# Kernel optimization log

Measured on AMD Instinct MI355X. Metric: run time of the kernel, lower is better.

Reference implementation:

```python
import jax, jax.numpy as jnp
import numpy as np

H = 32          # num_attention_heads
HD = 128        # head_dim
HID = H * HD    # hidden_size = 4096
KB_LEN = 1024   # number of KB entries
TOPK = 128      # top_k_kb (dynamic_sparsify=True)
ROPE_THETA = 10000.0
PAD = -1000000000.0  # PADDING_VALUE


def rope_cos_sin(position_ids, head_dim, theta):
    inv_freq = 1.0 / (theta ** (jnp.arange(0, head_dim, 2, dtype=jnp.float32) / head_dim))
    freqs = position_ids.astype(jnp.float32)[..., None] * inv_freq  # [B,q,hd/2]
    emb = jnp.concatenate([freqs, freqs], axis=-1)                  # [B,q,hd]
    return jnp.cos(emb), jnp.sin(emb)


def rotate_half(x):
    half = x.shape[-1] // 2
    return jnp.concatenate([-x[..., half:], x[..., :half]], axis=-1)


def apply_rope(q, k, cos, sin):
    cos = cos[:, None]  # [B,1,q,hd]
    sin = sin[:, None]
    return q * cos + rotate_half(q) * sin, k * cos + rotate_half(k) * sin


def setup_inputs() -> dict:
    key = jax.random.key(0)
    ks = jax.random.split(key, 9)
    B, Q = 1, 2048
    w_scale = 0.02  # keep activations numerically sane
    hidden_states = jax.random.normal(ks[0], (B, Q, HID), jnp.float32)
    causal = jnp.where(jnp.tril(jnp.ones((Q, Q), bool)), 0.0, PAD).astype(jnp.float32)
    attention_mask = jnp.broadcast_to(causal[None, None], (B, 1, Q, Q))
    position_ids = jnp.broadcast_to(jnp.arange(Q)[None], (B, Q))
    kb_keys = jax.random.normal(ks[1], (KB_LEN, HID), jnp.float32)
    kb_values = jax.random.normal(ks[2], (KB_LEN, HID), jnp.float32)
    Wq = jax.random.normal(ks[3], (HID, HID), jnp.float32) * w_scale
    Wq2 = jax.random.normal(ks[4], (HID, HID), jnp.float32) * w_scale
    Wk = jax.random.normal(ks[5], (HID, HID), jnp.float32) * w_scale
    Wv = jax.random.normal(ks[6], (HID, HID), jnp.float32) * w_scale
    Wo = jax.random.normal(ks[7], (HID, HID), jnp.float32) * w_scale
    score_shift = jnp.zeros((H, 1), jnp.float32) - 3.0
    return {"hidden_states": hidden_states, "attention_mask": attention_mask,
            "position_ids": position_ids, "kb_keys": kb_keys, "kb_values": kb_values,
            "Wq": Wq, "Wq2": Wq2, "Wk": Wk, "Wv": Wv, "Wo": Wo,
            "score_shift": score_shift}


def kblam_attention(hidden_states, attention_mask, position_ids, kb_keys, kb_values,
                    Wq, Wq2, Wk, Wv, Wo, score_shift):
    B, Q, _ = hidden_states.shape
    scale = 1.0 / np.sqrt(HD)

    def heads(x):  # [B,Q,HID] -> [B,H,Q,HD]
        return x.reshape(B, Q, H, HD).transpose(0, 2, 1, 3)

    q = heads(hidden_states @ Wq.T)
    q2 = heads(hidden_states @ Wq2.T)   # second query head (used for KB top-k pruning)
    k = heads(hidden_states @ Wk.T)
    v = heads(hidden_states @ Wv.T)

    cos, sin = rope_cos_sin(position_ids, HD, ROPE_THETA)
    q, k = apply_rope(q, k, cos, sin)   # num_kv_groups == 1, repeat_kv is identity

    # --- KB path: [kb_len, H*HD] -> [B,H,kb_len,HD] ---
    kbk = jnp.broadcast_to(kb_keys.reshape(KB_LEN, H, HD).transpose(1, 0, 2)[None], (B, H, KB_LEN, HD))
    kbv = jnp.broadcast_to(kb_values.reshape(KB_LEN, H, HD).transpose(1, 0, 2)[None], (B, H, KB_LEN, HD))

    # prune_key_value (dynamic_sparsify): top-k KB rows by summed q2-scores
    aw2 = jnp.einsum('bhqd,bhkd->bhqk', q2, kbk) * scale          # [B,H,Q,KB_LEN]
    idx = jax.lax.stop_gradient(jax.lax.top_k(aw2.sum((1, 2)), TOPK)[1])  # [B,TOPK]
    gidx = jnp.broadcast_to(idx[:, None, :, None], (B, H, TOPK, HD))
    kbk = jnp.take_along_axis(kbk, gidx, axis=2)                  # [B,H,TOPK,HD]
    kbv = jnp.take_along_axis(kbv, gidx, axis=2)
    kb_len = TOPK

    k_all = jnp.concatenate([kbk, k], axis=2)                     # [B,H,kb_len+Q,HD]
    v_all = jnp.concatenate([kbv, v], axis=2)

    # kb attention mask: zeros, except fully-padded query rows get PADDING_VALUE
    padding_mask = jnp.all(attention_mask < 0, axis=-1, keepdims=True)  # [B,1,Q,1]
    kb_mask = jnp.where(padding_mask, PAD, 0.0).astype(attention_mask.dtype)
    mask = jnp.concatenate([jnp.broadcast_to(kb_mask, (B, 1, Q, kb_len)), attention_mask], axis=-1)

    attn = jnp.einsum('bhqd,bhkd->bhqk', q, k_all) * scale
    # learned per-head shift on KB scores (score_shift: [H,1], init -3)
    attn = attn.at[..., :kb_len].add(score_shift.reshape(1, H, 1, 1))
    attn = attn + mask
    attn = jax.nn.softmax(attn.astype(jnp.float32), axis=-1).astype(q.dtype)

    out = jnp.einsum('bhqk,bhkd->bhqd', attn, v_all)              # [B,H,Q,HD]
    out = out.transpose(0, 2, 1, 3).reshape(B, Q, HID)
    return out @ Wo.T


def reference(hidden_states, attention_mask, position_ids, kb_keys, kb_values,
              Wq, Wq2, Wk, Wv, Wo, score_shift):
    return kblam_attention(hidden_states, attention_mask, position_ids, kb_keys, kb_values,
                           Wq, Wq2, Wk, Wv, Wo, score_shift)
```

## Files before the change

### kernel.cpp

```cpp
#include <hip/hip_runtime.h>
#include <stdint.h>
#include <stddef.h>

#define NH 32
#define HD 128
#define HID 4096
#define QLEN 2048
#define KBLEN 1024
#define NTOPK 128
#define KVLEN 2176
#define PADV -1e9f
#define SCALE 0.08838834764831845f
#define LOG2E 1.4426950408889634f
#define SC2 (SCALE * LOG2E)
#define DEFER_THR 8.0f

typedef __attribute__((ext_vector_type(4))) float f32x4;
typedef __attribute__((ext_vector_type(4))) unsigned short u16x4;
typedef __attribute__((ext_vector_type(8))) short s16x8;
typedef __attribute__((ext_vector_type(4))) short s16x4;

typedef const __attribute__((address_space(1))) void* gas1_t;
typedef __attribute__((address_space(3))) void* las3_t;

__device__ __forceinline__ void gload_lds16(const void* g, void* l) {
  __builtin_amdgcn_global_load_lds((gas1_t)g, (las3_t)l, 16, 0, 0);
}

__device__ __forceinline__ unsigned short f2bf(float x) {
  union { float f; unsigned u; } z; z.f = x;
  unsigned r = z.u + 0x7fffu + ((z.u >> 16) & 1u);
  return (unsigned short)(r >> 16);
}

__device__ __forceinline__ s16x4 tr16(unsigned addr) {
  s16x4 r;
  asm volatile("ds_read_b64_tr_b16 %0, %1" : "=v"(r) : "v"(addr));
  return r;
}

__device__ __forceinline__ s16x8 cat8(s16x4 a, s16x4 b) {
  s16x8 r;
  r[0]=a[0]; r[1]=a[1]; r[2]=a[2]; r[3]=a[3];
  r[4]=b[0]; r[5]=b[1]; r[6]=b[2]; r[7]=b[3];
  return r;
}


__global__ void k_cast(const float* __restrict__ src, unsigned short* __restrict__ dst, int n4) {
  int i = blockIdx.x * 256 + threadIdx.x;
  if (i >= n4) return;
  f32x4 v = ((const f32x4*)src)[i];
  u16x4 o;
  o[0] = f2bf(v[0]); o[1] = f2bf(v[1]); o[2] = f2bf(v[2]); o[3] = f2bf(v[3]);
  ((u16x4*)dst)[i] = o;
}

__global__ void k_rowsum_p(const float* __restrict__ x, float* __restrict__ part) {
  int d = blockIdx.x * 256 + threadIdx.x;
  int q0 = blockIdx.y * 128;
  float acc = 0.f;
  for (int q = q0; q < q0 + 128; ++q) acc += x[(size_t)q * HID + d];
  part[(size_t)blockIdx.y * HID + d] = acc;
}
__global__ void k_rowsum_r(const float* __restrict__ part, float* __restrict__ out) {
  int d = blockIdx.x * 256 + threadIdx.x;
  float acc = 0.f;
#pragma unroll
  for (int i = 0; i < 16; ++i) acc += part[(size_t)i * HID + d];
  out[d] = acc;
}

__global__ void k_dotrows(const float* __restrict__ vec, const float* __restrict__ mat,
                          float* __restrict__ out, int K, float s) {
  int n = blockIdx.x * 4 + (threadIdx.x >> 6);
  int lane = threadIdx.x & 63;
  const float* row = mat + (size_t)n * K;
  float acc = 0.f;
  for (int j = lane; j < K; j += 64) acc += vec[j] * row[j];
#pragma unroll
  for (int off = 32; off > 0; off >>= 1) acc += __shfl_down(acc, off, 64);
  if (lane == 0) out[n] = acc * s;
}

__global__ void k_topk(const float* __restrict__ scores, int* __restrict__ idx) {
  __shared__ float s[KBLEN];
  int t = threadIdx.x;
  s[t] = scores[t];
  __syncthreads();
  float mine = s[t];
  int rank = 0;
  for (int j = 0; j < KBLEN; ++j) {
    float v = s[j];
    rank += (v > mine) || (v == mine && j < t);
  }
  if (rank < NTOPK) idx[rank] = t;
}

__global__ void k_cs(const int* __restrict__ pos_ids, float2* __restrict__ cs) {
  int t = blockIdx.x * 256 + threadIdx.x;
  int p = t >> 6, i = t & 63;
  float pos = (float)pos_ids[p];
  float invf = powf(10000.0f, -(float)i / 64.0f);
  float a = pos * invf;
  cs[p * 64 + i] = make_float2(cosf(a), sinf(a));
}

__global__ void k_gather(const float* __restrict__ kbk, const float* __restrict__ kbv,
                         const int* __restrict__ idx,
                         unsigned short* __restrict__ kall, unsigned short* __restrict__ vall) {
  int t = blockIdx.x * 256 + threadIdx.x;
  int d = t & 127;
  int i = (t >> 7) & 127;
  int hh = t >> 14;
  int kr = idx[i];
  size_t src = (size_t)kr * HID + hh * HD + d;
  size_t dstoff = ((size_t)hh * KVLEN + i) * HD + d;
  kall[dstoff] = f2bf(kbk[src]);
  vall[dstoff] = f2bf(kbv[src]);
}

#define GBK 64
#define ABUF 8192
#define BBUF 16384
#define BUFE (ABUF + BBUF)

template<int MODE>
__global__ __launch_bounds__(512)
void gemm_bt(const unsigned short* __restrict__ A, const unsigned short* __restrict__ B,
             float* __restrict__ Cf, unsigned short* __restrict__ Cb,
             int M, int N, int K, int RH, int RO, const float2* __restrict__ cs2) {
  __shared__ unsigned short lds[3 * BUFE];
  const int tid = threadIdx.x;
  const int lane = tid & 63;
  const int wave = tid >> 6;
  const int lo = lane & 15, hi = lane >> 4;
  const int wm = wave >> 2, wn = wave & 3;

  const int nwg = gridDim.x * gridDim.y;
  const int orig = blockIdx.y * gridDim.x + blockIdx.x;
  const int wg = (orig & 7) * (nwg >> 3) + (orig >> 3);
  const int bx = wg % gridDim.x, by = wg / gridDim.x;
  const int m0 = by * 128, n0 = bx * 256;

  auto stageA = [&](int kt, int bufe, int g) {
    int j0 = g * 512 + wave * 64;
    int j = j0 + lane;
    int row = j >> 3, cb = j & 7;
    gload_lds16(A + (size_t)(m0 + row) * K + kt * GBK + ((cb ^ (row & 7)) << 3),
                (void*)(lds + bufe + j0 * 8));
  };
  auto stageB = [&](int kt, int bufe, int g) {
    int j0 = g * 512 + wave * 64;
    int j = j0 + lane;
    int row = j >> 3, cb = j & 7;
    gload_lds16(B + (size_t)(n0 + row) * K + kt * GBK + ((cb ^ (row & 7)) << 3),
                (void*)(lds + bufe + ABUF + j0 * 8));
  };

  f32x4 acc[4][4] = {};

  stageA(0, 0, 0); stageA(0, 0, 1);
  stageB(0, 0, 0); stageB(0, 0, 1); stageB(0, 0, 2); stageB(0, 0, 3);
  stageA(1, BUFE, 0); stageA(1, BUFE, 1);
  stageB(1, BUFE, 0); stageB(1, BUFE, 1); stageB(1, BUFE, 2); stageB(1, BUFE, 3);

  const int NT = K / GBK;
  const int sa = (lo & 7) << 3;
  const int bbase = (wn >> 1) * 128 + (wn & 1) * 32;
  int bi = 0;

  for (int kt = 0; kt < NT; ++kt) {
    if (kt < NT - 1) { asm volatile("s_waitcnt vmcnt(6)" ::: "memory"); }
    else             { asm volatile("s_waitcnt vmcnt(0)" ::: "memory"); }
    __builtin_amdgcn_sched_barrier(0);
    __builtin_amdgcn_s_barrier();
    __builtin_amdgcn_sched_barrier(0);

    const int bufe = bi * BUFE;
    const int nbufe = ((bi + 2 >= 3) ? bi - 1 : bi + 2) * BUFE;
    const bool pre = (kt + 2 < NT);
    const unsigned short* Ab = lds + bufe;
    const unsigned short* Bb = lds + bufe + ABUF;
    const int arow = wm * 64 + lo;
    const int brow = bbase + lo;

    s16x8 af[4], b01[2], b23[2];
    const int c0 = (hi * 8) ^ sa;
    const int c1 = (32 + hi * 8) ^ sa;

#pragma unroll
    for (int i = 0; i < 4; ++i) af[i] = *(const s16x8*)(Ab + (arow + i * 16) * 64 + c0);
    b01[0] = *(const s16x8*)(Bb + (brow +  0) * 64 + c0);
    b01[1] = *(const s16x8*)(Bb + (brow + 16) * 64 + c0);
    if (pre) { stageA(kt + 2, nbufe, 0); stageA(kt + 2, nbufe, 1); }
    asm volatile("s_waitcnt lgkmcnt(0)" ::: "memory");
    __builtin_amdgcn_sched_barrier(0);
    __builtin_amdgcn_s_setprio(1);
#pragma unroll
    for (int i = 0; i < 4; ++i) {
      acc[i][0] = __builtin_amdgcn_mfma_f32_16x16x32_bf16(af[i], b01[0], acc[i][0], 0, 0, 0);
      acc[i][1] = __builtin_amdgcn_mfma_f32_16x16x32_bf16(af[i], b01[1], acc[i][1], 0, 0, 0);
    }
    __builtin_amdgcn_s_setprio(0);

    b23[0] = *(const s16x8*)(Bb + (brow + 64) * 64 + c0);
    b23[1] = *(const s16x8*)(Bb + (brow + 80) * 64 + c0);
    if (pre) { stageB(kt + 2, nbufe, 0); stageB(kt + 2, nbufe, 1); }
    asm volatile("s_waitcnt lgkmcnt(0)" ::: "memory");
    __builtin_amdgcn_sched_barrier(0);
    __builtin_amdgcn_s_setprio(1);
#pragma unroll
    for (int i = 0; i < 4; ++i) {
      acc[i][2] = __builtin_amdgcn_mfma_f32_16x16x32_bf16(af[i], b23[0], acc[i][2], 0, 0, 0);
      acc[i][3] = __builtin_amdgcn_mfma_f32_16x16x32_bf16(af[i], b23[1], acc[i][3], 0, 0, 0);
    }
    __builtin_amdgcn_s_setprio(0);

#pragma unroll
    for (int i = 0; i < 4; ++i) af[i] = *(const s16x8*)(Ab + (arow + i * 16) * 64 + c1);
    b01[0] = *(const s16x8*)(Bb + (brow +  0) * 64 + c1);
    b01[1] = *(const s16x8*)(Bb + (brow + 16) * 64 + c1);
    if (pre) { stageB(kt + 2, nbufe, 2); stageB(kt + 2, nbufe, 3); }
    asm volatile("s_waitcnt lgkmcnt(0)" ::: "memory");
    __builtin_amdgcn_sched_barrier(0);
    __builtin_amdgcn_s_setprio(1);
#pragma unroll
    for (int i = 0; i < 4; ++i) {
      acc[i][0] = __builtin_amdgcn_mfma_f32_16x16x32_bf16(af[i], b01[0], acc[i][0], 0, 0, 0);
      acc[i][1] = __builtin_amdgcn_mfma_f32_16x16x32_bf16(af[i], b01[1], acc[i][1], 0, 0, 0);
    }
    __builtin_amdgcn_s_setprio(0);

    b23[0] = *(const s16x8*)(Bb + (brow + 64) * 64 + c1);
    b23[1] = *(const s16x8*)(Bb + (brow + 80) * 64 + c1);
    asm volatile("s_waitcnt lgkmcnt(0)" ::: "memory");
    __builtin_amdgcn_sched_barrier(0);
    __builtin_amdgcn_s_setprio(1);
#pragma unroll
    for (int i = 0; i < 4; ++i) {
      acc[i][2] = __builtin_amdgcn_mfma_f32_16x16x32_bf16(af[i], b23[0], acc[i][2], 0, 0, 0);
      acc[i][3] = __builtin_amdgcn_mfma_f32_16x16x32_bf16(af[i], b23[1], acc[i][3], 0, 0, 0);
    }
    __builtin_amdgcn_s_setprio(0);

    bi = (bi + 1 == 3) ? 0 : bi + 1;
  }

  if (MODE == 2) {
#pragma unroll
    for (int i = 0; i < 4; ++i) {
#pragma unroll
      for (int j = 0; j < 2; ++j) {
#pragma unroll
        for (int r = 0; r < 4; ++r) {
          int row = m0 + wm * 64 + i * 16 + hi * 4 + r;
          int col = n0 + bbase + j * 16 + lo;
          int hh = col >> 7, d = col & 127;
          float2 cp = cs2[row * 64 + d];
          float x1 = acc[i][j][r], x2 = acc[i][j + 2][r];
          size_t base = ((size_t)hh * RH + RO + row) * HD;
          Cb[base + d]      = f2bf(x1 * cp.x - x2 * cp.y);
          Cb[base + d + 64] = f2bf(x2 * cp.x + x1 * cp.y);
        }
      }
    }
  } else {
#pragma unroll
    for (int i = 0; i < 4; ++i) {
#pragma unroll
      for (int j = 0; j < 4; ++j) {
#pragma unroll
        for (int r = 0; r < 4; ++r) {
          int row = m0 + wm * 64 + i * 16 + hi * 4 + r;
          int col = n0 + bbase + (j >> 1) * 64 + (j & 1) * 16 + lo;
          float v = acc[i][j][r];
          if (MODE == 0) {
            Cf[(size_t)row * N + col] = v;
          } else {
            int hh = col >> 7, d = col & 127;
            Cb[((size_t)hh * RH + RO + row) * HD + d] = f2bf(v);
          }
        }
      }
    }
  }
}

__global__ __launch_bounds__(256)
void attn_kernel(const unsigned short* __restrict__ qh,
                 const unsigned short* __restrict__ kall,
                 const unsigned short* __restrict__ vall,
                 const float* __restrict__ sshift,
                 unsigned short* __restrict__ ctx) {
  __shared__ __align__(1024) unsigned short Ks[2][64 * 128];
  __shared__ __align__(1024) unsigned short Vs[2][64 * 128];
  __shared__ __align__(16)  unsigned short Plds[4][16 * 72];

  int orig = blockIdx.y * 16 + blockIdx.x;
  int wgid = (orig & 7) * 64 + (orig >> 3);
  int h = wgid >> 4;
  int xch = wgid & 15;

  const int tid = threadIdx.x;
  const int lane = tid & 63;
  const int wave = tid >> 6;
  const int lo = lane & 15;
  const int hi = lane >> 4;
  const float shiftL = sshift[h] * LOG2E;

  const unsigned short* kb = kall + (size_t)h * KVLEN * HD;
  const unsigned short* vb = vall + (size_t)h * KVLEN * HD;

#pragma unroll 1
  for (int half = 0; half < 2; ++half) {
    const int qc = half ? (31 - xch) : xch;
    const int m0 = qc * 64;

    s16x8 qf[4];
    {
      const unsigned short* qp = qh + ((size_t)h * QLEN + m0 + wave * 16 + lo) * HD + hi * 8;
#pragma unroll
      for (int kc = 0; kc < 4; ++kc) qf[kc] = *(const s16x8*)(qp + kc * 32);
    }

    float m_run[4], l_run[4];
#pragma unroll
    for (int r = 0; r < 4; ++r) { m_run[r] = -1e30f; l_run[r] = 0.f; }
    f32x4 o[8] = {};

    const int nt = qc + 3;
    const int qrow = m0 + wave * 16 + hi * 4;
    int buf = 0;

    auto STAGE = [&](int kt, int b) {
      const unsigned short* kg = kb + (size_t)kt * 64 * HD;
      const unsigned short* vg = vb + (size_t)kt * 64 * HD;
#pragma unroll
      for (int it = 0; it < 4; ++it) {
        int j0 = it * 256 + wave * 64;
        int j = j0 + lane;
        int row = j >> 4, cb = j & 15;
        gload_lds16(kg + row * 128 + ((cb ^ (row & 7)) * 8), (void*)(Ks[b] + j0 * 8));
        int kq = j >> 6, dc = (j >> 3) & 7, kr = (j >> 1) & 3, hf = j & 1;
        gload_lds16(vg + (kq * 4 + kr) * 128 + dc * 16 + hf * 8, (void*)(Vs[b] + j0 * 8));
      }
    };

    STAGE(0, 0);
    __syncthreads();

    for (int kt = 0; kt < nt; ++kt) {
      if (kt + 1 < nt) STAGE(kt + 1, buf ^ 1);

      f32x4 s[4] = {};
#pragma unroll
      for (int kc = 0; kc < 4; ++kc) {
#pragma unroll
        for (int g = 0; g < 4; ++g) {
          int key = g * 16 + lo;
          s16x8 kf = *(const s16x8*)(Ks[buf] + key * 128 + (((kc * 4 + hi) ^ (key & 7)) * 8));
          s[g] = __builtin_amdgcn_mfma_f32_16x16x32_bf16(qf[kc], kf, s[g], 0, 0, 0);
        }
      }

      const int kvbase = kt * 64;
      float sv[4][4], mx[4];
#pragma unroll
      for (int r = 0; r < 4; ++r) {
        int qr = qrow + r;
#pragma unroll
        for (int g = 0; g < 4; ++g) {
          int kv = kvbase + g * 16 + lo;
          float v = s[g][r] * SC2;
          v = (kv < NTOPK) ? (v + shiftL) : ((kv - NTOPK > qr) ? PADV : v);
          sv[g][r] = v;
        }
        mx[r] = fmaxf(fmaxf(sv[0][r], sv[1][r]), fmaxf(sv[2][r], sv[3][r]));
      }
#pragma unroll
      for (int off = 1; off < 16; off <<= 1)
#pragma unroll
        for (int r = 0; r < 4; ++r) mx[r] = fmaxf(mx[r], __shfl_xor(mx[r], off, 64));

      bool need = false;
#pragma unroll
      for (int r = 0; r < 4; ++r) need = need || (mx[r] > m_run[r] + DEFER_THR);
      if (need) {
#pragma unroll
        for (int r = 0; r < 4; ++r) {
          float mn = fmaxf(m_run[r], mx[r]);
          float alpha = __builtin_amdgcn_exp2f(m_run[r] - mn);
          m_run[r] = mn;
          l_run[r] *= alpha;
#pragma unroll
          for (int db = 0; db < 8; ++db) o[db][r] *= alpha;
        }
      }

      float rs[4];
#pragma unroll
      for (int r = 0; r < 4; ++r) {
        float acc = 0.f;
#pragma unroll
        for (int g = 0; g < 4; ++g) {
          float p = __builtin_amdgcn_exp2f(sv[g][r] - m_run[r]);
          acc += p;
          Plds[wave][(hi * 4 + r) * 72 + g * 16 + lo] = f2bf(p);
        }
        rs[r] = acc;
      }
#pragma unroll
      for (int off = 1; off < 16; off <<= 1)
#pragma unroll
        for (int r = 0; r < 4; ++r) rs[r] += __shfl_xor(rs[r], off, 64);
#pragma unroll
      for (int r = 0; r < 4; ++r) l_run[r] += rs[r];

      s16x8 pf0 = *(const s16x8*)(&Plds[wave][lo * 72 + hi * 8]);
      s16x8 pf1 = *(const s16x8*)(&Plds[wave][lo * 72 + 32 + hi * 8]);
      const unsigned vb0 = (unsigned)(uintptr_t)(&Vs[buf][0]) + hi * 2048 + lo * 8;
#pragma unroll
      for (int dbp = 0; dbp < 4; ++dbp) {
        s16x4 t[2][2][2];
#pragma unroll
        for (int dbi = 0; dbi < 2; ++dbi) {
          unsigned a0 = vb0 + (dbp * 2 + dbi) * 128;
          t[dbi][0][0] = tr16(a0);
          t[dbi][0][1] = tr16(a0 + 1024);
          t[dbi][1][0] = tr16(a0 + 8192);
          t[dbi][1][1] = tr16(a0 + 8192 + 1024);
        }
        asm volatile("s_waitcnt lgkmcnt(0)" ::: "memory");
        __builtin_amdgcn_sched_barrier(0);
#pragma unroll
        for (int dbi = 0; dbi < 2; ++dbi) {
          int db = dbp * 2 + dbi;
          o[db] = __builtin_amdgcn_mfma_f32_16x16x32_bf16(pf0, cat8(t[dbi][0][0], t[dbi][0][1]), o[db], 0, 0, 0);
          o[db] = __builtin_amdgcn_mfma_f32_16x16x32_bf16(pf1, cat8(t[dbi][1][0], t[dbi][1][1]), o[db], 0, 0, 0);
        }
      }

      __syncthreads();
      buf ^= 1;
    }

#pragma unroll
    for (int db = 0; db < 8; ++db) {
#pragma unroll
      for (int r = 0; r < 4; ++r) {
        int row = qrow + r;
        int col = h * HD + db * 16 + lo;
        ctx[(size_t)row * HID + col] = f2bf(o[db][r] / l_run[r]);
      }
    }
  }
}


extern "C" void kernel_launch(void* const* d_in, const int* in_sizes, int n_in,
                              void* d_out, int out_size, void* d_ws, size_t ws_size,
                              hipStream_t stream) {
  const float* hidden    = (const float*)d_in[0];
  const int*   pos       = (const int*)d_in[2];
  const float* kb_keys   = (const float*)d_in[3];
  const float* kb_values = (const float*)d_in[4];
  const float* Wq        = (const float*)d_in[5];
  const float* Wq2       = (const float*)d_in[6];
  const float* Wk        = (const float*)d_in[7];
  const float* Wv        = (const float*)d_in[8];
  const float* Wo        = (const float*)d_in[9];
  const float* sshift    = (const float*)d_in[10];
  float* out = (float*)d_out;

  char* ws = (char*)d_ws;
  size_t off = 0;
  auto alloc = [&](size_t bytes) { char* p = ws + off; off += (bytes + 255) & ~(size_t)255; return p; };
  unsigned short* hidden_bf = (unsigned short*)alloc((size_t)QLEN * HID * 2);
  unsigned short* wbuf      = (unsigned short*)alloc((size_t)HID * HID * 2);
  unsigned short* qbf       = (unsigned short*)alloc((size_t)NH * QLEN * HD * 2);
  unsigned short* kallp     = (unsigned short*)alloc((size_t)NH * KVLEN * HD * 2);
  unsigned short* vallp     = (unsigned short*)alloc((size_t)NH * KVLEN * HD * 2);
  unsigned short* ctx       = (unsigned short*)alloc((size_t)QLEN * HID * 2);
  float2*         cs2       = (float2*)alloc((size_t)QLEN * 64 * 8);
  float*          part      = (float*)alloc((size_t)16 * HID * 4);
  float*          hsum      = (float*)alloc(HID * 4);
  float*          qs        = (float*)alloc(HID * 4);
  float*          scores    = (float*)alloc(KBLEN * 4);
  int*            idx       = (int*)alloc(NTOPK * 4);

  dim3 blk(256);

  k_cast<<<QLEN * HID / 4 / 256, blk, 0, stream>>>(hidden, hidden_bf, QLEN * HID / 4);
  k_rowsum_p<<<dim3(HID / 256, 16), blk, 0, stream>>>(hidden, part);
  k_rowsum_r<<<HID / 256, blk, 0, stream>>>(part, hsum);
  k_dotrows<<<HID / 4, blk, 0, stream>>>(hsum, Wq2, qs, HID, 1.0f);
  k_dotrows<<<KBLEN / 4, blk, 0, stream>>>(qs, kb_keys, scores, HID, SCALE);
  k_topk<<<1, KBLEN, 0, stream>>>(scores, idx);
  k_cs<<<QLEN * 64 / 256, blk, 0, stream>>>(pos, cs2);

  dim3 ggrid(HID / 256, QLEN / 128);
  dim3 gblk(512);
  int wcast_blocks = HID * HID / 4 / 256;

  k_cast<<<wcast_blocks, blk, 0, stream>>>(Wq, wbuf, HID * HID / 4);
  gemm_bt<2><<<ggrid, gblk, 0, stream>>>(hidden_bf, wbuf, nullptr, qbf, QLEN, HID, HID, QLEN, 0, cs2);
  k_cast<<<wcast_blocks, blk, 0, stream>>>(Wk, wbuf, HID * HID / 4);
  gemm_bt<2><<<ggrid, gblk, 0, stream>>>(hidden_bf, wbuf, nullptr, kallp, QLEN, HID, HID, KVLEN, NTOPK, cs2);
  k_cast<<<wcast_blocks, blk, 0, stream>>>(Wv, wbuf, HID * HID / 4);
  gemm_bt<1><<<ggrid, gblk, 0, stream>>>(hidden_bf, wbuf, nullptr, vallp, QLEN, HID, HID, KVLEN, NTOPK, cs2);

  k_gather<<<NH * NTOPK * HD / 256, blk, 0, stream>>>(kb_keys, kb_values, idx, kallp, vallp);

  dim3 agrid(16, NH);
  attn_kernel<<<agrid, blk, 0, stream>>>(qbf, kallp, vallp, sshift, ctx);

  k_cast<<<wcast_blocks, blk, 0, stream>>>(Wo, wbuf, HID * HID / 4);
  gemm_bt<0><<<ggrid, gblk, 0, stream>>>(ctx, wbuf, out, nullptr, QLEN, HID, HID, 0, 0, cs2);
}
```

Measured before the change: 577.2 us.

## Store V transposed so attention reads B-fragments with plain LDS loads

The V projection GEMM and the KB gather now write V in a head-major transposed layout [H, HD, KVLEN]. The attention kernel stages V tiles into an XOR-swizzled LDS buffer and reads 16-byte fragments directly for the PV MFMA, replacing the ds_read_b64_tr_b16 transpose reads and their explicit waitcnt barriers. The V GEMM epilogue writes 4-element vectors along the sequence dimension. The gather's transposed V writes become strided, and the GEMM's transposed stores may coalesce worse.

```diff
diff --git a/kernel.cpp b/kernel.cpp
--- a/kernel.cpp
+++ b/kernel.cpp
@@ -18,7 +18,6 @@
 typedef __attribute__((ext_vector_type(4))) float f32x4;
 typedef __attribute__((ext_vector_type(4))) unsigned short u16x4;
 typedef __attribute__((ext_vector_type(8))) short s16x8;
-typedef __attribute__((ext_vector_type(4))) short s16x4;
 
 typedef const __attribute__((address_space(1))) void* gas1_t;
 typedef __attribute__((address_space(3))) void* las3_t;
@@ -31,19 +30,6 @@
   union { float f; unsigned u; } z; z.f = x;
   unsigned r = z.u + 0x7fffu + ((z.u >> 16) & 1u);
   return (unsigned short)(r >> 16);
-}
-
-__device__ __forceinline__ s16x4 tr16(unsigned addr) {
-  s16x4 r;
-  asm volatile("ds_read_b64_tr_b16 %0, %1" : "=v"(r) : "v"(addr));
-  return r;
-}
-
-__device__ __forceinline__ s16x8 cat8(s16x4 a, s16x4 b) {
-  s16x8 r;
-  r[0]=a[0]; r[1]=a[1]; r[2]=a[2]; r[3]=a[3];
-  r[4]=b[0]; r[5]=b[1]; r[6]=b[2]; r[7]=b[3];
-  return r;
 }
 
 
@@ -108,16 +94,15 @@
 
 __global__ void k_gather(const float* __restrict__ kbk, const float* __restrict__ kbv,
                          const int* __restrict__ idx,
-                         unsigned short* __restrict__ kall, unsigned short* __restrict__ vall) {
+                         unsigned short* __restrict__ kall, unsigned short* __restrict__ vallT) {
   int t = blockIdx.x * 256 + threadIdx.x;
   int d = t & 127;
   int i = (t >> 7) & 127;
   int hh = t >> 14;
   int kr = idx[i];
   size_t src = (size_t)kr * HID + hh * HD + d;
-  size_t dstoff = ((size_t)hh * KVLEN + i) * HD + d;
-  kall[dstoff] = f2bf(kbk[src]);
-  vall[dstoff] = f2bf(kbv[src]);
+  kall[((size_t)hh * KVLEN + i) * HD + d] = f2bf(kbk[src]);
+  vallT[((size_t)hh * HD + d) * KVLEN + i] = f2bf(kbv[src]);
 }
 
 #define GBK 64
@@ -265,6 +250,20 @@
         }
       }
     }
+  } else if (MODE == 3) {
+#pragma unroll
+    for (int i = 0; i < 4; ++i) {
+#pragma unroll
+      for (int j = 0; j < 4; ++j) {
+        int rowb = m0 + wm * 64 + i * 16 + hi * 4;
+        int col = n0 + bbase + (j >> 1) * 64 + (j & 1) * 16 + lo;
+        int hh = col >> 7, d = col & 127;
+        u16x4 o4;
+#pragma unroll
+        for (int r = 0; r < 4; ++r) o4[r] = f2bf(acc[i][j][r]);
+        *(u16x4*)(Cb + ((size_t)hh * HD + d) * RH + RO + rowb) = o4;
+      }
+    }
   } else {
 #pragma unroll
     for (int i = 0; i < 4; ++i) {
@@ -290,11 +289,11 @@
 __global__ __launch_bounds__(256)
 void attn_kernel(const unsigned short* __restrict__ qh,
                  const unsigned short* __restrict__ kall,
-                 const unsigned short* __restrict__ vall,
+                 const unsigned short* __restrict__ vallT,
                  const float* __restrict__ sshift,
                  unsigned short* __restrict__ ctx) {
   __shared__ __align__(1024) unsigned short Ks[2][64 * 128];
-  __shared__ __align__(1024) unsigned short Vs[2][64 * 128];
+  __shared__ __align__(1024) unsigned short Vs[2][128 * 64];
   __shared__ __align__(16)  unsigned short Plds[4][16 * 72];
 
   int orig = blockIdx.y * 16 + blockIdx.x;
@@ -310,7 +309,7 @@
   const float shiftL = sshift[h] * LOG2E;
 
   const unsigned short* kb = kall + (size_t)h * KVLEN * HD;
-  const unsigned short* vb = vall + (size_t)h * KVLEN * HD;
+  const unsigned short* vtb = vallT + (size_t)h * HD * KVLEN;
 
 #pragma unroll 1
   for (int half = 0; half < 2; ++half) {
@@ -335,15 +334,15 @@
 
     auto STAGE = [&](int kt, int b) {
       const unsigned short* kg = kb + (size_t)kt * 64 * HD;
-      const unsigned short* vg = vb + (size_t)kt * 64 * HD;
+      const unsigned short* vg = vtb + kt * 64;
 #pragma unroll
       for (int it = 0; it < 4; ++it) {
         int j0 = it * 256 + wave * 64;
         int j = j0 + lane;
         int row = j >> 4, cb = j & 15;
         gload_lds16(kg + row * 128 + ((cb ^ (row & 7)) * 8), (void*)(Ks[b] + j0 * 8));
-        int kq = j >> 6, dc = (j >> 3) & 7, kr = (j >> 1) & 3, hf = j & 1;
-        gload_lds16(vg + (kq * 4 + kr) * 128 + dc * 16 + hf * 8, (void*)(Vs[b] + j0 * 8));
+        int d = j >> 3, c = j & 7;
+        gload_lds16(vg + (size_t)d * KVLEN + ((c ^ (d & 7)) << 3), (void*)(Vs[b] + j0 * 8));
       }
     };
 
@@ -419,26 +418,14 @@
 
       s16x8 pf0 = *(const s16x8*)(&Plds[wave][lo * 72 + hi * 8]);
       s16x8 pf1 = *(const s16x8*)(&Plds[wave][lo * 72 + 32 + hi * 8]);
-      const unsigned vb0 = (unsigned)(uintptr_t)(&Vs[buf][0]) + hi * 2048 + lo * 8;
-#pragma unroll
-      for (int dbp = 0; dbp < 4; ++dbp) {
-        s16x4 t[2][2][2];
-#pragma unroll
-        for (int dbi = 0; dbi < 2; ++dbi) {
-          unsigned a0 = vb0 + (dbp * 2 + dbi) * 128;
-          t[dbi][0][0] = tr16(a0);
-          t[dbi][0][1] = tr16(a0 + 1024);
-          t[dbi][1][0] = tr16(a0 + 8192);
-          t[dbi][1][1] = tr16(a0 + 8192 + 1024);
-        }
-        asm volatile("s_waitcnt lgkmcnt(0)" ::: "memory");
-        __builtin_amdgcn_sched_barrier(0);
-#pragma unroll
-        for (int dbi = 0; dbi < 2; ++dbi) {
-          int db = dbp * 2 + dbi;
-          o[db] = __builtin_amdgcn_mfma_f32_16x16x32_bf16(pf0, cat8(t[dbi][0][0], t[dbi][0][1]), o[db], 0, 0, 0);
-          o[db] = __builtin_amdgcn_mfma_f32_16x16x32_bf16(pf1, cat8(t[dbi][1][0], t[dbi][1][1]), o[db], 0, 0, 0);
-        }
+      const unsigned short* Vb = Vs[buf];
+#pragma unroll
+      for (int db = 0; db < 8; ++db) {
+        int d = db * 16 + lo;
+        s16x8 vf0 = *(const s16x8*)(Vb + d * 64 + ((hi       ^ (d & 7)) << 3));
+        s16x8 vf1 = *(const s16x8*)(Vb + d * 64 + (((4 + hi) ^ (d & 7)) << 3));
+        o[db] = __builtin_amdgcn_mfma_f32_16x16x32_bf16(pf0, vf0, o[db], 0, 0, 0);
+        o[db] = __builtin_amdgcn_mfma_f32_16x16x32_bf16(pf1, vf1, o[db], 0, 0, 0);
       }
 
       __syncthreads();
@@ -480,7 +467,7 @@
   unsigned short* wbuf      = (unsigned short*)alloc((size_t)HID * HID * 2);
   unsigned short* qbf       = (unsigned short*)alloc((size_t)NH * QLEN * HD * 2);
   unsigned short* kallp     = (unsigned short*)alloc((size_t)NH * KVLEN * HD * 2);
-  unsigned short* vallp     = (unsigned short*)alloc((size_t)NH * KVLEN * HD * 2);
+  unsigned short* vallT     = (unsigned short*)alloc((size_t)NH * HD * KVLEN * 2);
   unsigned short* ctx       = (unsigned short*)alloc((size_t)QLEN * HID * 2);
   float2*         cs2       = (float2*)alloc((size_t)QLEN * 64 * 8);
   float*          part      = (float*)alloc((size_t)16 * HID * 4);
@@ -508,12 +495,12 @@
   k_cast<<<wcast_blocks, blk, 0, stream>>>(Wk, wbuf, HID * HID / 4);
   gemm_bt<2><<<ggrid, gblk, 0, stream>>>(hidden_bf, wbuf, nullptr, kallp, QLEN, HID, HID, KVLEN, NTOPK, cs2);
   k_cast<<<wcast_blocks, blk, 0, stream>>>(Wv, wbuf, HID * HID / 4);
-  gemm_bt<1><<<ggrid, gblk, 0, stream>>>(hidden_bf, wbuf, nullptr, vallp, QLEN, HID, HID, KVLEN, NTOPK, cs2);
-
-  k_gather<<<NH * NTOPK * HD / 256, blk, 0, stream>>>(kb_keys, kb_values, idx, kallp, vallp);
+  gemm_bt<3><<<ggrid, gblk, 0, stream>>>(hidden_bf, wbuf, nullptr, vallT, QLEN, HID, HID, KVLEN, NTOPK, cs2);
+
+  k_gather<<<NH * NTOPK * HD / 256, blk, 0, stream>>>(kb_keys, kb_values, idx, kallp, vallT);
 
   dim3 agrid(16, NH);
-  attn_kernel<<<agrid, blk, 0, stream>>>(qbf, kallp, vallp, sshift, ctx);
+  attn_kernel<<<agrid, blk, 0, stream>>>(qbf, kallp, vallT, sshift, ctx);
 
   k_cast<<<wcast_blocks, blk, 0, stream>>>(Wo, wbuf, HID * HID / 4);
   gemm_bt<0><<<ggrid, gblk, 0, stream>>>(ctx, wbuf, out, nullptr, QLEN, HID, HID, 0, 0, cs2);
```

Result: slower. 617.4 us (+7.0%).
